# Optimization experiments

Hardware: AMD Instinct MI355X
Metric: run time of the kernel (lower is better)

The kernel has to match this reference:

```python
import jax, jax.numpy as jnp
import numpy as np

EMB_DIM, TREE_DIM, OUT_DIM, VOCAB = 256, 256, 3, 10000
T, B, LEVELS = 255, 128, 8  # complete binary tree of depth 8, 128 trees per input


def _build_forest():
    # node j = T-1-heap(j): root (heap 0) is the LAST node so stack_last_h picks the root.
    heap = np.arange(T)
    depth = np.floor(np.log2(heap + 1)).astype(np.int64)  # 0..7
    node_order = np.empty(T, dtype=np.int64)
    node_order[T - 1 - heap] = (LEVELS - 1) - depth       # leaves=0, root=7
    internal = np.arange((T - 1) // 2)                     # heaps with two children
    parent = np.repeat(T - 1 - internal, 2)
    child = np.stack([T - 1 - (2 * internal + 1), T - 1 - (2 * internal + 2)], 1).reshape(-1)
    edges = np.stack([parent, child], axis=1)              # (254, 2)
    edge_order = node_order[parent]
    offs = (np.arange(B) * T)[:, None, None]
    adj = (edges[None] + offs).reshape(-1, 2)              # (B*254, 2)
    return np.tile(node_order, B), adj, np.tile(edge_order, B)


def setup_inputs() -> dict:
    key = jax.random.key(0)
    ks = jax.random.split(key, 16)
    no, adj, eo = _build_forest()
    D = TREE_DIM
    s_e = 1.0 / np.sqrt(EMB_DIM)
    s_t = 1.0 / np.sqrt(D)
    return {
        'feat_cube': jax.random.randint(ks[0], (B * T,), 0, VOCAB),
        'feat_a': jax.random.randint(ks[1], (B * T,), 0, VOCAB),
        'feat_b': jax.random.randint(ks[2], (B * T,), 0, VOCAB),
        'node_order': jnp.asarray(no),
        'adjacency_list': jnp.asarray(adj),
        'edge_order': jnp.asarray(eo),
        'num_levels': LEVELS,
        'num_trees': B,
        'emb': jax.random.normal(ks[3], (VOCAB, EMB_DIM), jnp.float32),
        'W_iou': jax.random.normal(ks[4], (3 * D, EMB_DIM), jnp.float32) * s_e,
        'b_iou': jnp.zeros((3 * D,), jnp.float32),
        'U_iou': jax.random.normal(ks[5], (3 * D, D), jnp.float32) * s_t,
        'W_f': jax.random.normal(ks[6], (D, EMB_DIM), jnp.float32) * s_e,
        'b_f': jnp.zeros((D,), jnp.float32),
        'U_f': jax.random.normal(ks[7], (D, D), jnp.float32) * s_t,
        'fc1_w': jax.random.normal(ks[8], (D // 2, D), jnp.float32) * s_t,
        'fc1_b': jnp.zeros((D // 2,), jnp.float32),
        'fc2_w': jax.random.normal(ks[9], (OUT_DIM, D // 2), jnp.float32) * (1.0 / np.sqrt(D // 2)),
        'fc2_b': jnp.zeros((OUT_DIM,), jnp.float32),
    }


def _tree_lstm(x, node_order, parents, children, edge_order, W_iou, b_iou, U_iou, W_f, b_f, U_f, num_levels):
    # Child-sum TreeLSTM, evaluated level by level (leaves first). Dense masked
    # formulation: per level we update only nodes with node_order==lvl; edge
    # contributions are masked before segment_sum (same math as the torch loop).
    N = x.shape[0]
    D = U_f.shape[0]
    x_iou = x @ W_iou.T + b_iou            # (N, 3D), precomputed once
    x_f = x @ W_f.T + b_f                  # (N, D)
    h = jnp.zeros((N, D), x.dtype)
    c = jnp.zeros((N, D), x.dtype)
    for lvl in range(num_levels):
        emask = (edge_order == lvl)[:, None].astype(x.dtype)
        ch = h[children]                   # (E, D) gather of child hidden
        cc = c[children]
        f = jax.nn.sigmoid(x_f[parents] + ch @ U_f.T)
        h_sum = jax.ops.segment_sum(ch * emask, parents, num_segments=N)
        c_sum = jax.ops.segment_sum(f * cc * emask, parents, num_segments=N)
        i, o, u = jnp.split(x_iou + h_sum @ U_iou.T, 3, axis=1)
        c_new = jax.nn.sigmoid(i) * jnp.tanh(u) + c_sum
        h_new = jax.nn.sigmoid(o) * jnp.tanh(c_new)
        nmask = (node_order == lvl)[:, None]
        h = jnp.where(nmask, h_new, h)
        c = jnp.where(nmask, c_new, c)
    return h, c


def reference(feat_cube, feat_a, feat_b, node_order, adjacency_list, edge_order,
              num_levels, num_trees, emb, W_iou, b_iou, U_iou, W_f, b_f, U_f,
              fc1_w, fc1_b, fc2_w, fc2_b):
    parents = adjacency_list[:, 0]
    children = adjacency_list[:, 1]

    def run_tree(feat):
        h, _ = _tree_lstm(emb[feat], node_order, parents, children, edge_order,
                          W_iou, b_iou, U_iou, W_f, b_f, U_f, num_levels)
        # stack_last_h: last node of each tree (= root with our labeling)
        return h.reshape(num_trees, -1, h.shape[-1])[:, -1, :]

    h_c = run_tree(feat_cube)
    h_a = run_tree(feat_a)
    h_b = run_tree(feat_b)
    # h_c (1,D) @ (h_a (D,1) @ h_b (1,D)) == (h_c . h_a) * h_b, fused einsum
    h = jnp.einsum('bi,bi,bj->bj', h_c, h_a, h_b)
    hid = jax.nn.relu(h @ fc1_w.T + fc1_b)
    logits = jax.nn.relu(hid @ fc2_w.T + fc2_b)
    return logits  # (num_trees, out_dim)
```

## Files before the change

kernel.cpp:

```cpp
#include <hip/hip_runtime.h>
#include <hip/hip_bf16.h>

typedef __hip_bfloat16 bf16;
typedef unsigned short u16;
typedef __attribute__((ext_vector_type(8))) short s8;
typedef __attribute__((ext_vector_type(4))) float f4;

#define NRUNS 3
#define NTREE 128
#define TT    255
#define DD    256
#define VPAD  10016
#define PAD   258
#define OPAD  264

__device__ __forceinline__ float bits2f(u16 b){ union{unsigned u; float f;} x; x.u = ((unsigned)b)<<16; return x.f; }
__device__ __forceinline__ u16   f2bits(float f){ bf16 h = __float2bfloat16(f); return *(u16*)&h; }
__device__ __forceinline__ float sigm(float x){ return 1.f/(1.f+__expf(-x)); }
__device__ __forceinline__ float tanh_(float x){ return 1.f - 2.f/(__expf(2.f*x)+1.f); }

__global__ void k_detect(const u16* __restrict__ raw, int* __restrict__ flag){
    int t = threadIdx.x;
    int hit = 0;
    if (t < 128){
        u16 w = raw[2*t];
        int e = (w >> 7) & 0xFF;
        hit = (e >= 100 && e <= 141) ? 1 : 0;
    }
    __shared__ int cnt;
    if (t == 0) cnt = 0;
    __syncthreads();
    atomicAdd(&cnt, hit);
    __syncthreads();
    if (t == 0) flag[0] = (cnt >= 64) ? 1 : 0;
}

__device__ __forceinline__ u16 cvt1b(const void* p, int i, int isb){
    return isb ? ((const u16*)p)[i] : f2bits(((const float*)p)[i]);
}
__device__ __forceinline__ float cvt1f(const void* p, int i, int isb){
    return isb ? bits2f(((const u16*)p)[i]) : ((const float*)p)[i];
}

#define L_EMB  (10000*256)
#define L_EMBP (VPAD*256)
#define L_WIOU (768*256)
#define L_UIOU (768*256)
#define L_WF   (256*256)
#define L_UF   (256*256)
#define L_ALL  (L_EMBP + L_WIOU + L_UIOU + L_WF + L_UF)
__global__ void k_cvtb(const void* __restrict__ s0, const void* __restrict__ s1,
                       const void* __restrict__ s2, const void* __restrict__ s3,
                       const void* __restrict__ s4,
                       u16* __restrict__ d0, u16* __restrict__ d1, u16* __restrict__ d2,
                       u16* __restrict__ d3, u16* __restrict__ d4,
                       const int* __restrict__ flag){
    int isb = flag[0];
    for (int i = blockIdx.x*blockDim.x + threadIdx.x; i < L_ALL; i += gridDim.x*blockDim.x){
        int j = i;
        if (j < L_EMBP){ d0[j] = (j < L_EMB) ? cvt1b(s0, j, isb) : (u16)0; continue; } j -= L_EMBP;
        if (j < L_WIOU){ d1[j] = cvt1b(s1, j, isb); continue; } j -= L_WIOU;
        if (j < L_UIOU){ d2[j] = cvt1b(s2, j, isb); continue; } j -= L_UIOU;
        if (j < L_WF){ d3[j] = cvt1b(s3, j, isb); continue; } j -= L_WF;
        d4[j] = cvt1b(s4, j, isb);
    }
}

#define S_BIOU 768
#define S_BF   256
#define S_F1W  (128*256)
#define S_F1B  128
#define S_F2W  (3*128)
#define S_F2B  3
#define S_ALL  (S_BIOU+S_BF+S_F1W+S_F1B+S_F2W+S_F2B)
__global__ void k_small(const void* __restrict__ s0, const void* __restrict__ s1,
                        const void* __restrict__ s2, const void* __restrict__ s3,
                        const void* __restrict__ s4, const void* __restrict__ s5,
                        float* __restrict__ d0, float* __restrict__ d1, float* __restrict__ d2,
                        float* __restrict__ d3, float* __restrict__ d4, float* __restrict__ d5,
                        const int* __restrict__ flag){
    int isb = flag[0];
    for (int i = blockIdx.x*blockDim.x + threadIdx.x; i < S_ALL; i += gridDim.x*blockDim.x){
        int j = i;
        if (j < S_BIOU){ d0[j] = cvt1f(s0, j, isb); continue; } j -= S_BIOU;
        if (j < S_BF){ d1[j] = cvt1f(s1, j, isb); continue; } j -= S_BF;
        if (j < S_F1W){ d2[j] = cvt1f(s2, j, isb); continue; } j -= S_F1W;
        if (j < S_F1B){ d3[j] = cvt1f(s3, j, isb); continue; } j -= S_F1B;
        if (j < S_F2W){ d4[j] = cvt1f(s4, j, isb); continue; } j -= S_F2W;
        d5[j] = cvt1f(s5, j, isb);
    }
}

__device__ __forceinline__ s8 ldB16(const u16* p){
    union { uint4 q; s8 v; } u;
    u.q = *(const uint4*)p;
    return u.v;
}
__device__ __forceinline__ s8 ldsA(const u16* p){
    union { unsigned w[4]; s8 v; } u;
    u.w[0] = *(const unsigned*)(p);
    u.w[1] = *(const unsigned*)(p+2);
    u.w[2] = *(const unsigned*)(p+4);
    u.w[3] = *(const unsigned*)(p+6);
    return u.v;
}
#define MFMA(acc,a,b) acc = __builtin_amdgcn_mfma_f32_16x16x32_bf16(a, b, acc, 0, 0, 0)

__global__ __launch_bounds__(512, 4)
void k_vocab2(const u16* __restrict__ embb,
              const u16* __restrict__ Wiou, const u16* __restrict__ Wfm,
              const u16* __restrict__ Ufm,  const float* __restrict__ biou_f,
              u16* __restrict__ E4, u16* __restrict__ E_f,
              u16* __restrict__ H0, u16* __restrict__ C0, u16* __restrict__ HU0)
{
    __shared__ u16 hs[32*PAD];
    const int t = threadIdx.x, w = t>>6, lane = t&63, ln = lane&15, q = lane>>4;
    const int r0 = blockIdx.x*32, d0 = w*32;

    const u16* Bp[8];
    #pragma unroll
    for (int g = 0; g < 4; g++)
      #pragma unroll
      for (int nc = 0; nc < 2; nc++){
        int nn = d0 + nc*16 + ln;
        Bp[g*2+nc] = (g < 3) ? (Wiou + (size_t)(g*256+nn)*DD) : (Wfm + (size_t)nn*DD);
      }
    const u16* a0p = embb + (size_t)(r0+ln)*DD;
    const u16* a1p = embb + (size_t)(r0+16+ln)*DD;
    f4 acc[8][2];
    #pragma unroll
    for (int nt = 0; nt < 8; nt++){ acc[nt][0] = (f4){0,0,0,0}; acc[nt][1] = (f4){0,0,0,0}; }
    #pragma unroll 2
    for (int ks = 0; ks < 8; ks++){
        int ko = ks*32 + q*8;
        s8 a0 = ldB16(a0p + ko);
        s8 a1 = ldB16(a1p + ko);
        #pragma unroll
        for (int nt = 0; nt < 8; nt++){
            s8 bb = ldB16(Bp[nt] + ko);
            MFMA(acc[nt][0], a0, bb);
            MFMA(acc[nt][1], a1, bb);
        }
    }
    #pragma unroll
    for (int nc = 0; nc < 2; nc++){
        int d = d0 + nc*16 + ln;
        float bi = biou_f[d], bo = biou_f[256+d], bu = biou_f[512+d];
        #pragma unroll
        for (int ms = 0; ms < 2; ms++)
          #pragma unroll
          for (int r = 0; r < 4; r++){
            int vrow = r0 + ms*16 + q*4 + r;
            float ei = acc[0*2+nc][ms][r];
            float eo = acc[1*2+nc][ms][r];
            float eu = acc[2*2+nc][ms][r];
            float ef = acc[3*2+nc][ms][r];
            union { u16 a[4]; uint2 q2; } pk;
            pk.a[0] = f2bits(ei);
            pk.a[1] = f2bits(eo);
            pk.a[2] = f2bits(eu);
            pk.a[3] = f2bits(ef);
            *(uint2*)(E4 + ((size_t)vrow*DD + d)*4) = pk.q2;
            E_f[(size_t)vrow*DD + d] = f2bits(ef);
            float cc = sigm(ei + bi)*tanh_(eu + bu);
            float hh = sigm(eo + bo)*tanh_(cc);
            C0[(size_t)vrow*DD + d] = f2bits(cc);
            H0[(size_t)vrow*DD + d] = f2bits(hh);
            hs[(ms*16 + q*4 + r)*PAD + d] = f2bits(hh);
        }
    }
    __syncthreads();

    f4 hacc[2][2];
    #pragma unroll
    for (int nt = 0; nt < 2; nt++){ hacc[nt][0] = (f4){0,0,0,0}; hacc[nt][1] = (f4){0,0,0,0}; }
    const u16* Bf0 = Ufm + (size_t)(d0 + ln)*DD;
    const u16* Bf1 = Ufm + (size_t)(d0 + 16 + ln)*DD;
    #pragma unroll 2
    for (int ks = 0; ks < 8; ks++){
        int ko = ks*32 + q*8;
        s8 a0 = ldsA(&hs[ln*PAD + ko]);
        s8 a1 = ldsA(&hs[(16+ln)*PAD + ko]);
        s8 b0 = ldB16(Bf0 + ko);
        s8 b1 = ldB16(Bf1 + ko);
        MFMA(hacc[0][0], a0, b0); MFMA(hacc[0][1], a1, b0);
        MFMA(hacc[1][0], a0, b1); MFMA(hacc[1][1], a1, b1);
    }
    #pragma unroll
    for (int nc = 0; nc < 2; nc++){
        int d = d0 + nc*16 + ln;
        #pragma unroll
        for (int ms = 0; ms < 2; ms++)
          #pragma unroll
          for (int r = 0; r < 4; r++){
            int vrow = r0 + ms*16 + q*4 + r;
            HU0[(size_t)vrow*DD + d] = f2bits(hacc[nc][ms][r]);
        }
    }
}

__global__ __launch_bounds__(512, 4)
void k_edge0(const int* __restrict__ f0, const int* __restrict__ f1, const int* __restrict__ f2,
             const u16* __restrict__ E_f, const u16* __restrict__ H0,
             const u16* __restrict__ C0,  const u16* __restrict__ HU0,
             const float* __restrict__ bf_f,
             u16* __restrict__ hsum_out, u16* __restrict__ fcsum_out)
{
    int gid = blockIdx.x*512 + threadIdx.x;
    int row = gid >> 5, ch = gid & 31, d = ch*8;
    int run = row >> 13, rem = row & 8191, b = rem >> 6, jj = rem & 63;
    const int* fp = (run==0) ? f0 : ((run==1) ? f1 : f2);
    int fo = fp[b*TT + 128 + jj];
    int v1 = fp[b*TT + 2*jj];
    int v2 = fp[b*TT + 2*jj + 1];
    s8 ef  = ldB16(E_f + (size_t)fo*DD + d);
    s8 hu1 = ldB16(HU0 + (size_t)v1*DD + d);
    s8 hu2 = ldB16(HU0 + (size_t)v2*DD + d);
    s8 c1  = ldB16(C0  + (size_t)v1*DD + d);
    s8 c2  = ldB16(C0  + (size_t)v2*DD + d);
    s8 h1  = ldB16(H0  + (size_t)v1*DD + d);
    s8 h2  = ldB16(H0  + (size_t)v2*DD + d);
    union { u16 a[8]; uint4 q4; } uh, uf;
    #pragma unroll
    for (int j = 0; j < 8; j++){
        float e  = bits2f((u16)ef[j]) + bf_f[d+j];
        float fa = sigm(e + bits2f((u16)hu1[j]));
        float fb = sigm(e + bits2f((u16)hu2[j]));
        float fc = fa*bits2f((u16)c1[j]) + fb*bits2f((u16)c2[j]);
        float hsv = bits2f((u16)h1[j]) + bits2f((u16)h2[j]);
        uf.a[j] = f2bits(fc);
        uh.a[j] = f2bits(hsv);
    }
    *(uint4*)(hsum_out  + (size_t)row*DD + d) = uh.q4;
    *(uint4*)(fcsum_out + (size_t)row*DD + d) = uf.q4;
}

__global__ __launch_bounds__(512, 3)
void k_lvl(int lvl, int cLog,
           const int* __restrict__ f0, const int* __restrict__ f1, const int* __restrict__ f2,
           const u16* __restrict__ E4, const u16* __restrict__ E_f,
           const u16* __restrict__ Uiou, const u16* __restrict__ Ufm,
           const float* __restrict__ biou_f, const float* __restrict__ bf_f,
           const u16* __restrict__ hsum_in, const u16* __restrict__ fcsum_in,
           u16* __restrict__ hsum_out, u16* __restrict__ fcsum_out,
           u16* __restrict__ hroot)
{
    __shared__ u16 hs[32*PAD];
    __shared__ u16 hso[16*OPAD];
    __shared__ u16 fco[16*OPAD];
    __shared__ int sfr[32];
    const int t = threadIdx.x, w = t>>6, lane = t&63, ln = lane&15, q = lane>>4;
    const int cnt = 1 << cLog, S = 256 - 2*cnt;
    const int r0 = blockIdx.x*32, d0 = w*32;
    const bool haveP = (lvl < 7);

    if (t < 32){
        int rho = r0 + t;
        int run = rho >> (7+cLog);
        int rem = rho & ((1<<(7+cLog)) - 1);
        int b = rem >> cLog, jj = rem & (cnt-1);
        const int* fp = (run==0) ? f0 : ((run==1) ? f1 : f2);
        sfr[t] = fp[b*TT + S + jj];
    }

    int featp[2][2];
    if (haveP){
        #pragma unroll
        for (int ms = 0; ms < 2; ms++)
          #pragma unroll
          for (int rr = 0; rr < 2; rr++){
            int rho = r0 + ms*16 + q*4 + rr*2;
            int run = rho >> (7+cLog);
            int rem = rho & ((1<<(7+cLog)) - 1);
            int b = rem >> cLog, jj = rem & (cnt-1);
            const int* fp = (run==0) ? f0 : ((run==1) ? f1 : f2);
            featp[ms][rr] = fp[b*TT + (256-cnt) + (jj>>1)];
          }
    }
    __syncthreads();

    uint2 epf[2][2][4];
    #pragma unroll
    for (int nc = 0; nc < 2; nc++){
        int d = d0 + nc*16 + ln;
        #pragma unroll
        for (int ms = 0; ms < 2; ms++)
          #pragma unroll
          for (int r = 0; r < 4; r++){
            int m = ms*16 + q*4 + r;
            epf[nc][ms][r] = *(const uint2*)(E4 + ((size_t)sfr[m]*DD + d)*4);
          }
    }

    f4 acc[6][2];
    #pragma unroll
    for (int nt = 0; nt < 6; nt++){ acc[nt][0] = (f4){0,0,0,0}; acc[nt][1] = (f4){0,0,0,0}; }
    {
        const u16* a0p = hsum_in + (size_t)(r0+ln)*DD;
        const u16* a1p = hsum_in + (size_t)(r0+16+ln)*DD;
        const u16* Bp[6];
        #pragma unroll
        for (int nt = 0; nt < 6; nt++){
            int n = (nt>>1)*256 + d0 + (nt&1)*16 + ln;
            Bp[nt] = Uiou + (size_t)n*DD;
        }
        #pragma unroll 2
        for (int ks = 0; ks < 8; ks++){
            int ko = ks*32 + q*8;
            s8 a0 = ldB16(a0p + ko);
            s8 a1 = ldB16(a1p + ko);
            #pragma unroll
            for (int nt = 0; nt < 6; nt++){
                s8 bb = ldB16(Bp[nt] + ko);
                MFMA(acc[nt][0], a0, bb);
                MFMA(acc[nt][1], a1, bb);
            }
        }
    }

    float cv[2][2][4];
    #pragma unroll
    for (int nc = 0; nc < 2; nc++){
        int d = d0 + nc*16 + ln;
        float bi = biou_f[d], bo = biou_f[256+d], bu = biou_f[512+d];
        #pragma unroll
        for (int ms = 0; ms < 2; ms++){
            float hv[4];
            #pragma unroll
            for (int r = 0; r < 4; r++){
                int m   = ms*16 + q*4 + r;
                int rho = r0 + m;
                union { uint2 q2; u16 a[4]; } ev;
                ev.q2 = epf[nc][ms][r];
                float iv = acc[0+nc][ms][r] + bits2f(ev.a[0]) + bi;
                float ov = acc[2+nc][ms][r] + bits2f(ev.a[1]) + bo;
                float uv = acc[4+nc][ms][r] + bits2f(ev.a[2]) + bu;
                float cs = bits2f(fcsum_in[(size_t)rho*DD + d]);
                float c = sigm(iv)*tanh_(uv) + cs;
                float h = sigm(ov)*tanh_(c);
                cv[nc][ms][r] = c;
                hv[r] = h;
                if (haveP) hs[m*PAD + d] = f2bits(h);
                else       hroot[(size_t)rho*DD + d] = f2bits(h);
            }
            if (haveP){
                int lr = ms*8 + q*2;
                hso[lr*OPAD + d]     = f2bits(hv[0] + hv[1]);
                hso[(lr+1)*OPAD + d] = f2bits(hv[2] + hv[3]);
            }
        }
    }

    if (haveP){
        __syncthreads();
        f4 hacc[2][2];
        #pragma unroll
        for (int nt = 0; nt < 2; nt++){ hacc[nt][0] = (f4){0,0,0,0}; hacc[nt][1] = (f4){0,0,0,0}; }
        const u16* Bf0 = Ufm + (size_t)(d0 + ln)*DD;
        const u16* Bf1 = Ufm + (size_t)(d0 + 16 + ln)*DD;
        #pragma unroll 2
        for (int ks = 0; ks < 8; ks++){
            int ko = ks*32 + q*8;
            s8 a0 = ldsA(&hs[ln*PAD + ko]);
            s8 a1 = ldsA(&hs[(16+ln)*PAD + ko]);
            s8 b0 = ldB16(Bf0 + ko);
            s8 b1 = ldB16(Bf1 + ko);
            MFMA(hacc[0][0], a0, b0); MFMA(hacc[0][1], a1, b0);
            MFMA(hacc[1][0], a0, b1); MFMA(hacc[1][1], a1, b1);
        }
        #pragma unroll
        for (int nc = 0; nc < 2; nc++){
            int d = d0 + nc*16 + ln;
            float bfv = bf_f[d];
            #pragma unroll
            for (int ms = 0; ms < 2; ms++){
                float fs0, fs1;
                #pragma unroll
                for (int r = 0; r < 4; r++){
                    float ef = bits2f(E_f[(size_t)featp[ms][r>>1]*DD + d]);
                    float fc = sigm(ef + bfv + hacc[nc][ms][r]) * cv[nc][ms][r];
                    if (r == 0) fs0 = fc;
                    else if (r == 1) fs0 += fc;
                    else if (r == 2) fs1 = fc;
                    else fs1 += fc;
                }
                int lr = ms*8 + q*2;
                fco[lr*OPAD + d]     = f2bits(fs0);
                fco[(lr+1)*OPAD + d] = f2bits(fs1);
            }
        }

        __syncthreads();
        {
            int row = t >> 5, c = (t & 31) * 8;
            int prow = (r0 >> 1) + row;
            uint4 vh = *(const uint4*)&hso[row*OPAD + c];
            uint4 vf = *(const uint4*)&fco[row*OPAD + c];
            *(uint4*)(hsum_out  + (size_t)prow*DD + c) = vh;
            *(uint4*)(fcsum_out + (size_t)prow*DD + c) = vf;
        }
    }
}

__global__ __launch_bounds__(256)
void k_final(const u16* __restrict__ hroot,
             const float* __restrict__ fc1w, const float* __restrict__ fc1b,
             const float* __restrict__ fc2w, const float* __restrict__ fc2b,
             void* __restrict__ out, const int* __restrict__ flag)
{
    int b = blockIdx.x, t = threadIdx.x;
    __shared__ float sprod[DD];
    __shared__ float shb[DD];
    __shared__ float shid[128];
    float hc  = bits2f(hroot[(0*NTREE + b)*DD + t]);
    float ha  = bits2f(hroot[(1*NTREE + b)*DD + t]);
    float hbv = bits2f(hroot[(2*NTREE + b)*DD + t]);
    sprod[t] = hc * ha;
    shb[t]   = hbv;
    __syncthreads();
    for (int s = 128; s > 0; s >>= 1){
        if (t < s) sprod[t] += sprod[t + s];
        __syncthreads();
    }
    float dot = sprod[0];
    if (t < 128){
        float acc = fc1b[t];
        for (int k = 0; k < DD; k++)
            acc = fmaf(dot * shb[k], fc1w[t*DD + k], acc);
        shid[t] = fmaxf(acc, 0.f);
    }
    __syncthreads();
    if (t < 3){
        float acc = fc2b[t];
        for (int j = 0; j < 128; j++)
            acc = fmaf(fc2w[t*128 + j], shid[j], acc);
        float v = fmaxf(acc, 0.f);
        if (flag[0]) ((bf16*)out)[b*3 + t] = __float2bfloat16(v);
        else         ((float*)out)[b*3 + t] = v;
    }
}

extern "C" void kernel_launch(void* const* d_in, const int* in_sizes, int n_in,
                              void* d_out, int out_size, void* d_ws, size_t ws_size,
                              hipStream_t stream)
{
    const int* f0 = (const int*)d_in[0];
    const int* f1 = (const int*)d_in[1];
    const int* f2 = (const int*)d_in[2];
    const void* emb  = d_in[8];
    const void* Wiou = d_in[9];
    const void* biou = d_in[10];
    const void* Uiou = d_in[11];
    const void* Wf   = d_in[12];
    const void* bfv  = d_in[13];
    const void* Uf   = d_in[14];
    const void* fc1w = d_in[15];
    const void* fc1b = d_in[16];
    const void* fc2w = d_in[17];
    const void* fc2b = d_in[18];

    char* base = (char*)d_ws;
    size_t off = 0;
    auto take = [&](size_t bytes) -> char* {
        char* p = base + off;
        off = (off + bytes + 255) & ~(size_t)255;
        return p;
    };
    int*   flag   = (int*)  take(256);
    u16*   embb   = (u16*)  take((size_t)L_EMBP*2);
    u16*   wioub  = (u16*)  take((size_t)L_WIOU*2);
    u16*   uioub  = (u16*)  take((size_t)L_UIOU*2);
    u16*   wfb    = (u16*)  take((size_t)L_WF*2);
    u16*   ufb    = (u16*)  take((size_t)L_UF*2);
    float* biou_f = (float*)take(S_BIOU*4);
    float* bf_f   = (float*)take(S_BF*4);
    float* fc1w_f = (float*)take(S_F1W*4);
    float* fc1b_f = (float*)take(S_F1B*4);
    float* fc2w_f = (float*)take(S_F2W*4);
    float* fc2b_f = (float*)take(S_F2B*4);
    u16*   E4     = (u16*)  take((size_t)VPAD*DD*4*2);
    u16*   E_f    = (u16*)  take((size_t)VPAD*DD*2);
    u16*   H0     = (u16*)  take((size_t)VPAD*DD*2);
    u16*   C0     = (u16*)  take((size_t)VPAD*DD*2);
    u16*   HU0    = (u16*)  take((size_t)VPAD*DD*2);
    u16*   HA     = (u16*)  take((size_t)24576*DD*2);
    u16*   HB     = (u16*)  take((size_t)12288*DD*2);
    u16*   FA     = (u16*)  take((size_t)24576*DD*2);
    u16*   FB     = (u16*)  take((size_t)12288*DD*2);
    u16*   hroot  = (u16*)  take((size_t)NRUNS*NTREE*DD*2);

    k_detect<<<1, 256, 0, stream>>>((const u16*)emb, flag);
    k_cvtb<<<2048, 256, 0, stream>>>(emb, Wiou, Uiou, Wf, Uf,
                                     embb, wioub, uioub, wfb, ufb, flag);
    k_small<<<135, 256, 0, stream>>>(biou, bfv, fc1w, fc1b, fc2w, fc2b,
                                     biou_f, bf_f, fc1w_f, fc1b_f, fc2w_f, fc2b_f, flag);
    k_vocab2<<<VPAD/32, 512, 0, stream>>>(embb, wioub, wfb, ufb, biou_f,
                                          E4, E_f, H0, C0, HU0);
    k_edge0<<<24576*32/512, 512, 0, stream>>>(f0, f1, f2, E_f, H0, C0, HU0, bf_f, HA, FA);

    for (int lvl = 1; lvl <= 7; lvl++){
        int cLog = 7 - lvl;
        int rows = NRUNS*NTREE*(128 >> lvl);
        int blocks = rows / 32;
        int pe = lvl & 1;
        u16* hs_o = pe ? HB : HA;
        u16* fc_o = pe ? FB : FA;
        const u16* hs_i = pe ? HA : HB;
        const u16* fc_i = pe ? FA : FB;
        k_lvl<<<blocks, 512, 0, stream>>>(lvl, cLog, f0, f1, f2,
                                          E4, E_f, uioub, ufb,
                                          biou_f, bf_f,
                                          hs_i, fc_i, hs_o, fc_o, hroot);
    }
    k_final<<<NTREE, 256, 0, stream>>>(hroot, fc1w_f, fc1b_f, fc2w_f, fc2b_f, d_out, flag);
}
```

Measured before the change: 464.8 us.

## Fuse tree levels 4-7 into one kernel keeping parent state in LDS

Replaces the four per-level launches for the upper tree levels with a single k_tail kernel. Each block handles four complete subtrees and keeps the intermediate h-sum and forget-c-sum in double-buffered shared memory, so levels 4-7 need no global round-trips or launch gaps. The E4 prefetch in k_lvl is moved into the epilogue and launch bounds are raised to 4 blocks per CU to cut register pressure. In exchange the upper levels run with partially empty 32-row MFMA tiles and only 96 blocks, and k_tail uses more shared memory.

After: 432.8 us. -6.9%, faster.

```diff
diff --git a/kernel.cpp b/kernel.cpp
--- a/kernel.cpp
+++ b/kernel.cpp
@@ -13,6 +13,7 @@
 #define VPAD  10016
 #define PAD   258
 #define OPAD  264
+#define FPAD  264
 
 __device__ __forceinline__ float bits2f(u16 b){ union{unsigned u; float f;} x; x.u = ((unsigned)b)<<16; return x.f; }
 __device__ __forceinline__ u16   f2bits(float f){ bf16 h = __float2bfloat16(f); return *(u16*)&h; }
@@ -235,7 +236,7 @@
     *(uint4*)(fcsum_out + (size_t)row*DD + d) = uf.q4;
 }
 
-__global__ __launch_bounds__(512, 3)
+__global__ __launch_bounds__(512, 4)
 void k_lvl(int lvl, int cLog,
            const int* __restrict__ f0, const int* __restrict__ f1, const int* __restrict__ f2,
            const u16* __restrict__ E4, const u16* __restrict__ E_f,
@@ -279,19 +280,6 @@
     }
     __syncthreads();
 
-    uint2 epf[2][2][4];
-    #pragma unroll
-    for (int nc = 0; nc < 2; nc++){
-        int d = d0 + nc*16 + ln;
-        #pragma unroll
-        for (int ms = 0; ms < 2; ms++)
-          #pragma unroll
-          for (int r = 0; r < 4; r++){
-            int m = ms*16 + q*4 + r;
-            epf[nc][ms][r] = *(const uint2*)(E4 + ((size_t)sfr[m]*DD + d)*4);
-          }
-    }
-
     f4 acc[6][2];
     #pragma unroll
     for (int nt = 0; nt < 6; nt++){ acc[nt][0] = (f4){0,0,0,0}; acc[nt][1] = (f4){0,0,0,0}; }
@@ -331,7 +319,7 @@
                 int m   = ms*16 + q*4 + r;
                 int rho = r0 + m;
                 union { uint2 q2; u16 a[4]; } ev;
-                ev.q2 = epf[nc][ms][r];
+                ev.q2 = *(const uint2*)(E4 + ((size_t)sfr[m]*DD + d)*4);
                 float iv = acc[0+nc][ms][r] + bits2f(ev.a[0]) + bi;
                 float ov = acc[2+nc][ms][r] + bits2f(ev.a[1]) + bo;
                 float uv = acc[4+nc][ms][r] + bits2f(ev.a[2]) + bu;
@@ -398,6 +386,164 @@
             uint4 vf = *(const uint4*)&fco[row*OPAD + c];
             *(uint4*)(hsum_out  + (size_t)prow*DD + c) = vh;
             *(uint4*)(fcsum_out + (size_t)prow*DD + c) = vf;
+        }
+    }
+}
+
+__global__ __launch_bounds__(512, 4)
+void k_tail(const int* __restrict__ f0, const int* __restrict__ f1, const int* __restrict__ f2,
+            const u16* __restrict__ E4, const u16* __restrict__ E_f,
+            const u16* __restrict__ Uiou, const u16* __restrict__ Ufm,
+            const float* __restrict__ biou_f, const float* __restrict__ bf_f,
+            const u16* __restrict__ hsum_in, const u16* __restrict__ fcsum_in,
+            u16* __restrict__ hroot)
+{
+    __shared__ u16 hs[32*PAD];
+    __shared__ u16 hsP[2][32*PAD];
+    __shared__ u16 fcP[2][32*FPAD];
+    __shared__ int sf[64];
+    const int t = threadIdx.x, w = t>>6, lane = t&63, ln = lane&15, q = lane>>4;
+    const int d0 = w*32;
+    const int r0 = blockIdx.x*32;
+    const int run = (blockIdx.x*4) >> 7;
+    const int* __restrict__ fp = (run==0) ? f0 : ((run==1) ? f1 : f2);
+
+    if (t < 64){
+        int ti = t >> 4, idx = t & 15;
+        int b = (blockIdx.x*4 + ti) & 127;
+        sf[t] = (idx < 15) ? fp[b*TT + 240 + idx] : 0;
+    }
+    __syncthreads();
+
+    const u16* Bp[6];
+    #pragma unroll
+    for (int nt = 0; nt < 6; nt++){
+        int n = (nt>>1)*256 + d0 + (nt&1)*16 + ln;
+        Bp[nt] = Uiou + (size_t)n*DD;
+    }
+    const u16* Bf0 = Ufm + (size_t)(d0 + ln)*DD;
+    const u16* Bf1 = Ufm + (size_t)(d0 + 16 + ln)*DD;
+
+    for (int l = 4; l <= 7; l++){
+        const int nl = 128 >> l;
+        const int nrows = 4*nl;
+        const int sh = 7 - l;
+        const int inb = (l-1) & 1, outb = l & 1;
+        const bool haveP = (l < 7);
+
+        f4 acc[6][2];
+        #pragma unroll
+        for (int nt = 0; nt < 6; nt++){ acc[nt][0] = (f4){0,0,0,0}; acc[nt][1] = (f4){0,0,0,0}; }
+        if (l == 4){
+            const u16* a0p = hsum_in + (size_t)(r0+ln)*DD;
+            const u16* a1p = hsum_in + (size_t)(r0+16+ln)*DD;
+            #pragma unroll 2
+            for (int ks = 0; ks < 8; ks++){
+                int ko = ks*32 + q*8;
+                s8 a0 = ldB16(a0p + ko);
+                s8 a1 = ldB16(a1p + ko);
+                #pragma unroll
+                for (int nt = 0; nt < 6; nt++){
+                    s8 bb = ldB16(Bp[nt] + ko);
+                    MFMA(acc[nt][0], a0, bb);
+                    MFMA(acc[nt][1], a1, bb);
+                }
+            }
+        } else {
+            const u16* a0l = &hsP[inb][ln*PAD];
+            const u16* a1l = &hsP[inb][(16+ln)*PAD];
+            #pragma unroll 2
+            for (int ks = 0; ks < 8; ks++){
+                int ko = ks*32 + q*8;
+                s8 a0 = ldsA(a0l + ko);
+                s8 a1 = ldsA(a1l + ko);
+                #pragma unroll
+                for (int nt = 0; nt < 6; nt++){
+                    s8 bb = ldB16(Bp[nt] + ko);
+                    MFMA(acc[nt][0], a0, bb);
+                    MFMA(acc[nt][1], a1, bb);
+                }
+            }
+        }
+
+        float cv[2][2][4];
+        #pragma unroll
+        for (int nc = 0; nc < 2; nc++){
+            int d = d0 + nc*16 + ln;
+            float bi = biou_f[d], bo = biou_f[256+d], bu = biou_f[512+d];
+            #pragma unroll
+            for (int ms = 0; ms < 2; ms++){
+                float hv[4];
+                #pragma unroll
+                for (int r = 0; r < 4; r++){
+                    int m = ms*16 + q*4 + r;
+                    bool vld = (m < nrows);
+                    int mc = vld ? m : 0;
+                    int ti = mc >> sh, jj = mc & (nl-1);
+                    int fidx = sf[ti*16 + (16 - 2*nl) + jj];
+                    union { uint2 q2; u16 a[4]; } ev;
+                    ev.q2 = *(const uint2*)(E4 + ((size_t)fidx*DD + d)*4);
+                    float iv = acc[0+nc][ms][r] + bits2f(ev.a[0]) + bi;
+                    float ov = acc[2+nc][ms][r] + bits2f(ev.a[1]) + bo;
+                    float uv = acc[4+nc][ms][r] + bits2f(ev.a[2]) + bu;
+                    float cs = (l == 4) ? bits2f(fcsum_in[(size_t)(r0+m)*DD + d])
+                                        : bits2f(fcP[inb][m*FPAD + d]);
+                    float c = sigm(iv)*tanh_(uv) + cs;
+                    float h = sigm(ov)*tanh_(c);
+                    cv[nc][ms][r] = c;
+                    hv[r] = h;
+                    if (haveP) hs[m*PAD + d] = f2bits(h);
+                    else if (vld) hroot[(size_t)(blockIdx.x*4 + m)*DD + d] = f2bits(h);
+                }
+                if (haveP){
+                    int lr = ms*8 + q*2;
+                    hsP[outb][lr*PAD + d]     = f2bits(hv[0] + hv[1]);
+                    hsP[outb][(lr+1)*PAD + d] = f2bits(hv[2] + hv[3]);
+                }
+            }
+        }
+
+        if (haveP){
+            __syncthreads();
+            f4 hacc[2][2];
+            #pragma unroll
+            for (int nt = 0; nt < 2; nt++){ hacc[nt][0] = (f4){0,0,0,0}; hacc[nt][1] = (f4){0,0,0,0}; }
+            #pragma unroll 2
+            for (int ks = 0; ks < 8; ks++){
+                int ko = ks*32 + q*8;
+                s8 a0 = ldsA(&hs[ln*PAD + ko]);
+                s8 a1 = ldsA(&hs[(16+ln)*PAD + ko]);
+                s8 b0 = ldB16(Bf0 + ko);
+                s8 b1 = ldB16(Bf1 + ko);
+                MFMA(hacc[0][0], a0, b0); MFMA(hacc[0][1], a1, b0);
+                MFMA(hacc[1][0], a0, b1); MFMA(hacc[1][1], a1, b1);
+            }
+            #pragma unroll
+            for (int nc = 0; nc < 2; nc++){
+                int d = d0 + nc*16 + ln;
+                float bfv = bf_f[d];
+                #pragma unroll
+                for (int ms = 0; ms < 2; ms++){
+                    float fs0, fs1;
+                    #pragma unroll
+                    for (int r = 0; r < 4; r++){
+                        int m2 = ms*16 + q*4 + (r & 2);
+                        int mc2 = (m2 < nrows) ? m2 : 0;
+                        int ti2 = mc2 >> sh, jj2 = mc2 & (nl-1);
+                        int fpar = sf[ti2*16 + (16 - nl) + (jj2 >> 1)];
+                        float ef = bits2f(E_f[(size_t)fpar*DD + d]);
+                        float fc = sigm(ef + bfv + hacc[nc][ms][r]) * cv[nc][ms][r];
+                        if (r == 0) fs0 = fc;
+                        else if (r == 1) fs0 += fc;
+                        else if (r == 2) fs1 = fc;
+                        else fs1 += fc;
+                    }
+                    int lr = ms*8 + q*2;
+                    fcP[outb][lr*FPAD + d]     = f2bits(fs0);
+                    fcP[outb][(lr+1)*FPAD + d] = f2bits(fs1);
+                }
+            }
+            __syncthreads();
         }
     }
 }
@@ -498,7 +644,7 @@
                                           E4, E_f, H0, C0, HU0);
     k_edge0<<<24576*32/512, 512, 0, stream>>>(f0, f1, f2, E_f, H0, C0, HU0, bf_f, HA, FA);
 
-    for (int lvl = 1; lvl <= 7; lvl++){
+    for (int lvl = 1; lvl <= 3; lvl++){
         int cLog = 7 - lvl;
         int rows = NRUNS*NTREE*(128 >> lvl);
         int blocks = rows / 32;
@@ -512,5 +658,7 @@
                                           biou_f, bf_f,
                                           hs_i, fc_i, hs_o, fc_o, hroot);
     }
+    k_tail<<<(NRUNS*NTREE)/4, 512, 0, stream>>>(f0, f1, f2, E4, E_f, uioub, ufb,
+                                                biou_f, bf_f, HB, FB, hroot);
     k_final<<<NTREE, 256, 0, stream>>>(hroot, fc1w_f, fc1b_f, fc2w_f, fc2b_f, d_out, flag);
 }
```
